# Optimization experiments

Hardware: AMD Instinct MI355X
Metric: run time of the kernel (lower is better)

The kernel has to match this reference:

```python
import jax, jax.numpy as jnp
import numpy as np

EPS_DIST = 1e-10
BN_EPS = 1e-5
K = 3  # nsample / three_nn


def setup_inputs() -> dict:
    key = jax.random.key(0)
    ks = jax.random.split(key, 8)
    B, N, S, D1, D2 = 4, 8192, 2048, 128, 256
    C_in = D1 + D2  # 384
    H = 256
    inp = {
        "pos1": jax.random.normal(ks[0], (B, 3, N), dtype=jnp.float32),
        "pos2": jax.random.normal(ks[1], (B, 3, S), dtype=jnp.float32),
        "feature1": jax.random.normal(ks[2], (B, D1, N), dtype=jnp.float32),
        "feature2": jax.random.normal(ks[3], (B, D2, S), dtype=jnp.float32),
        # MLP layer 1: Conv1d(384->256, k=1) + BN
        "W1": jax.random.normal(ks[4], (H, C_in), dtype=jnp.float32) * (1.0 / np.sqrt(C_in)),
        "b1": jnp.zeros((H,), dtype=jnp.float32),
        "g1": jnp.ones((H,), dtype=jnp.float32),
        "be1": jnp.zeros((H,), dtype=jnp.float32),
        # MLP layer 2: Conv1d(256->256, k=1) + BN
        "W2": jax.random.normal(ks[5], (H, H), dtype=jnp.float32) * (1.0 / np.sqrt(H)),
        "b2": jnp.zeros((H,), dtype=jnp.float32),
        "g2": jnp.ones((H,), dtype=jnp.float32),
        "be2": jnp.zeros((H,), dtype=jnp.float32),
    }
    return inp


def _conv_bn_relu(x, W, b, gamma, beta):
    # x: [B, Cin, N]; 1x1 Conv1d == channel GEMM
    y = jnp.einsum("oc,bcn->bon", W, x) + b[None, :, None]
    # BatchNorm1d in training mode: batch statistics over (B, N)
    mean = jnp.mean(y, axis=(0, 2), keepdims=True)
    var = jnp.mean(jnp.square(y - mean), axis=(0, 2), keepdims=True)
    y = (y - mean) * jax.lax.rsqrt(var + BN_EPS)
    y = y * gamma[None, :, None] + beta[None, :, None]
    return jax.nn.relu(y)


def reference(pos1, pos2, feature1, feature2, W1, b1, g1, be1, W2, b2, g2, be2):
    # pos1: [B,3,N], pos2: [B,3,S], feature1: [B,D1,N], feature2: [B,D2,S]
    p1 = jnp.swapaxes(pos1, 1, 2)  # [B,N,3]
    p2 = jnp.swapaxes(pos2, 1, 2)  # [B,S,3]
    # three_nn: squared-distance 3-NN of each point in p1 among p2
    d2 = (jnp.sum(p1 * p1, -1)[:, :, None]
          + jnp.sum(p2 * p2, -1)[:, None, :]
          - 2.0 * jnp.einsum("bnc,bsc->bns", p1, p2))  # [B,N,S]
    neg_vals, idx = jax.lax.top_k(-d2, K)  # idx: [B,N,3]
    dists = jnp.maximum(-neg_vals, EPS_DIST)  # dists[dists<1e-10]=1e-10
    w = 1.0 / dists
    w = w / jnp.sum(w, -1, keepdims=True)  # [B,N,3]
    # grouping_operation: gather feature2 [B,D,S] by idx -> [B,D,N,3]
    grouped = jax.vmap(lambda f, i: f[:, i])(feature2, idx)
    interpolated = jnp.sum(grouped * w[:, None, :, :], axis=-1)  # [B,D2,N]
    feat = jnp.concatenate([interpolated, feature1], axis=1)  # [B,384,N]
    feat = _conv_bn_relu(feat, W1, b1, g1, be1)
    feat = _conv_bn_relu(feat, W2, b2, g2, be2)
    return feat  # [B,256,N]
```

## Files before the change

### kernel.cpp

```cpp
#include <hip/hip_runtime.h>
#include <hip/hip_bf16.h>
#include <cstdint>

typedef unsigned short u16;
typedef unsigned int u32;
typedef unsigned long long u64;
typedef __bf16 bf16x8 __attribute__((ext_vector_type(8)));
typedef float f32x4 __attribute__((ext_vector_type(4)));

__device__ __forceinline__ u16 f2b(float f) {
    unsigned int u = __float_as_uint(f);
    u += 0x7fffu + ((u >> 16) & 1u);
    return (u16)(u >> 16);
}
__device__ __forceinline__ float b2f(u16 h) {
    return __uint_as_float(((unsigned int)h) << 16);
}
__device__ __forceinline__ void async_cp16(void* lds, const void* g) {
    __builtin_amdgcn_global_load_lds((const __attribute__((address_space(1))) void*)g,
                                     (__attribute__((address_space(3))) void*)lds, 16, 0, 0);
}
__device__ __forceinline__ u32 fmono(float f) {
    u32 u = __float_as_uint(f);
    return u ^ (((u32)((int)u >> 31)) | 0x80000000u);
}
__device__ __forceinline__ u64 shfl_xor_u64(u64 v, int mask) {
    u32 lo = (u32)v, hi = (u32)(v >> 32);
    lo = (u32)__shfl_xor((int)lo, mask);
    hi = (u32)__shfl_xor((int)hi, mask);
    return ((u64)hi << 32) | lo;
}
__device__ __forceinline__ void ins3(u64 k, u64& k0, u64& k1, u64& k2) {
    bool c0 = k > k0, c1 = k > k1, c2 = k > k2;
    k2 = c1 ? k1 : (c2 ? k : k2);
    k1 = c0 ? k0 : (c1 ? k : k1);
    k0 = c0 ? k : k0;
}
__device__ __forceinline__ int pkix(int i) { return i + (i >> 7); }

#define NB_NN  1024
#define NB_CVT 160
#define NB_T2  512
#define NB_T1  1024

__global__ __launch_bounds__(256, 8) void prep_kernel(const float* __restrict__ w1,
                                                      const float* __restrict__ w2,
                                                      u16* __restrict__ wb,
                                                      const float* __restrict__ feature2,
                                                      u16* __restrict__ f2t,
                                                      const float* __restrict__ feature1,
                                                      u16* __restrict__ f1t,
                                                      const float* __restrict__ pos1,
                                                      const float* __restrict__ pos2,
                                                      int* __restrict__ idx_out,
                                                      float* __restrict__ w_out) {
    __shared__ __align__(16) char smem[19712];
    int bi = blockIdx.x;
    int tid = threadIdx.x;

    if (bi >= NB_NN) {
        int ci = bi - NB_NN;
        if (ci < NB_CVT) {
            int i = ci * 256 + tid;
            if (i < 40960) {
                const float* src = (i < 24576) ? w1 : w2;
                int k = (i < 24576) ? i : (i - 24576);
                float4 v = *(const float4*)&src[(size_t)k * 4];
                ushort4 o;
                o.x = f2b(v.x); o.y = f2b(v.y); o.z = f2b(v.z); o.w = f2b(v.w);
                *(ushort4*)&wb[(size_t)i * 4] = o;
            }
            return;
        }
        float (*t)[65] = (float (*)[65])smem;
        const float* in; u16* out; int C, S, s0, c0, b;
        if (ci < NB_CVT + NB_T2) {
            int lin = ci - NB_CVT;
            C = 256; S = 2048; in = feature2; out = f2t;
            s0 = (lin & 31) * 64; c0 = ((lin >> 5) & 3) * 64; b = lin >> 7;
        } else {
            int lin = ci - NB_CVT - NB_T2;
            C = 128; S = 8192; in = feature1; out = f1t;
            s0 = (lin & 127) * 64; c0 = ((lin >> 7) & 1) * 64; b = lin >> 8;
        }
        const float* ib = in + (size_t)b * C * S;
        u16* ob = out + (size_t)b * S * C;
        int col = tid & 63, r0 = tid >> 6;
#pragma unroll
        for (int p = 0; p < 16; ++p) {
            int c = p * 4 + r0;
            t[c][col] = ib[(size_t)(c0 + c) * S + s0 + col];
        }
        __syncthreads();
#pragma unroll
        for (int p = 0; p < 16; ++p) {
            int s = p * 4 + r0;
            ob[(size_t)(s0 + s) * C + c0 + col] = f2b(t[col][s]);
        }
        return;
    }

    float4* pk = (float4*)smem;
    u64* warr = (u64*)(smem + 16512);
    int j0 = bi * 32;
    int b = j0 >> 13;
    const float* p2 = pos2 + (size_t)b * 3 * 2048;
    int p = tid & 15, ck = tid >> 4;
    int wv = tid >> 6, lane = tid & 63;
    int na = (j0 & 8191) + p, nbq = na + 16;
    const float* p1 = pos1 + (size_t)b * 3 * 8192;
    float xa = p1[na], ya = p1[8192 + na], za = p1[16384 + na];
    float xb = p1[nbq], yb = p1[8192 + nbq], zb = p1[16384 + nbq];

    u64 a0k = 0, a1k = 0, a2k = 0, b0k = 0, b1k = 0, b2k = 0;

    for (int half = 0; half < 2; ++half) {
        int hbase = half * 1024;
        for (int i = tid; i < 1024; i += 256) {
            int s = hbase + i;
            float x = p2[s], y = p2[2048 + s], z = p2[4096 + s];
            pk[pkix(i)] = make_float4(x, y, z, -0.5f * (x * x + y * y + z * z));
        }
        __syncthreads();

        float ga0 = -3.4e38f, ga1 = -3.4e38f, ga2 = -3.4e38f;
        float gb0 = -3.4e38f, gb1 = -3.4e38f, gb2 = -3.4e38f;
        int ia0 = 0, ia1 = 0, ia2 = 0, ib0 = 0, ib1 = 0, ib2 = 0;
        int sb = ck * 64;
        const float4* pc = pk + pkix(sb);
#pragma unroll 4
        for (int it = 0; it < 64; ++it) {
            float4 cd = pc[it];
            int s = sb + it;
            float ta = fmaf(xa, cd.x, fmaf(ya, cd.y, fmaf(za, cd.z, cd.w)));
            float tb = fmaf(xb, cd.x, fmaf(yb, cd.y, fmaf(zb, cd.z, cd.w)));
            bool a0 = ta > ga0, a1 = ta > ga1, a2 = ta > ga2;
            ga2 = a1 ? ga1 : (a2 ? ta : ga2);
            ia2 = a1 ? ia1 : (a2 ? s : ia2);
            ga1 = a0 ? ga0 : (a1 ? ta : ga1);
            ia1 = a0 ? ia0 : (a1 ? s : ia1);
            ga0 = a0 ? ta : ga0;
            ia0 = a0 ? s : ia0;
            bool b0c = tb > gb0, b1c = tb > gb1, b2c = tb > gb2;
            gb2 = b1c ? gb1 : (b2c ? tb : gb2);
            ib2 = b1c ? ib1 : (b2c ? s : ib2);
            gb1 = b0c ? gb0 : (b1c ? tb : gb1);
            ib1 = b0c ? ib0 : (b1c ? s : ib1);
            gb0 = b0c ? tb : gb0;
            ib0 = b0c ? s : ib0;
        }
        __syncthreads();

        int gi0 = hbase + ia0, gi1 = hbase + ia1, gi2 = hbase + ia2;
        int gj0 = hbase + ib0, gj1 = hbase + ib1, gj2 = hbase + ib2;
        ins3(((u64)fmono(ga0) << 32) | (u64)(2047 - gi0), a0k, a1k, a2k);
        ins3(((u64)fmono(ga1) << 32) | (u64)(2047 - gi1), a0k, a1k, a2k);
        ins3(((u64)fmono(ga2) << 32) | (u64)(2047 - gi2), a0k, a1k, a2k);
        ins3(((u64)fmono(gb0) << 32) | (u64)(2047 - gj0), b0k, b1k, b2k);
        ins3(((u64)fmono(gb1) << 32) | (u64)(2047 - gj1), b0k, b1k, b2k);
        ins3(((u64)fmono(gb2) << 32) | (u64)(2047 - gj2), b0k, b1k, b2k);
    }

#pragma unroll
    for (int mask = 16; mask <= 32; mask <<= 1) {
        u64 pa0 = shfl_xor_u64(a0k, mask), pa1 = shfl_xor_u64(a1k, mask), pa2 = shfl_xor_u64(a2k, mask);
        u64 pb0 = shfl_xor_u64(b0k, mask), pb1 = shfl_xor_u64(b1k, mask), pb2 = shfl_xor_u64(b2k, mask);
        ins3(pa0, a0k, a1k, a2k); ins3(pa1, a0k, a1k, a2k); ins3(pa2, a0k, a1k, a2k);
        ins3(pb0, b0k, b1k, b2k); ins3(pb1, b0k, b1k, b2k); ins3(pb2, b0k, b1k, b2k);
    }
    if (lane < 16) {
        u64* wr = &warr[(wv * 16 + p) * 6];
        wr[0] = a0k; wr[1] = a1k; wr[2] = a2k;
        wr[3] = b0k; wr[4] = b1k; wr[5] = b2k;
    }
    __syncthreads();
    if (tid < 32) {
        int q = tid;
        int pp = q & 15, off = (q < 16) ? 0 : 3;
        const u64* w0 = &warr[pp * 6];
        u64 k0 = w0[off], k1 = w0[off + 1], k2 = w0[off + 2];
#pragma unroll
        for (int w = 1; w < 4; ++w) {
            const u64* wr = &warr[(w * 16 + pp) * 6];
            ins3(wr[off], k0, k1, k2);
            ins3(wr[off + 1], k0, k1, k2);
            ins3(wr[off + 2], k0, k1, k2);
        }
        int s0 = 2047 - (int)(k0 & 0xFFFFFFFFu);
        int s1 = 2047 - (int)(k1 & 0xFFFFFFFFu);
        int s2 = 2047 - (int)(k2 & 0xFFFFFFFFu);
        int j = j0 + q;
        int n = j & 8191;
        float x1 = p1[n], y1 = p1[8192 + n], z1 = p1[16384 + n];
        float n1 = x1 * x1 + y1 * y1 + z1 * z1;
        float X0 = p2[s0], Y0 = p2[2048 + s0], Z0 = p2[4096 + s0];
        float X1 = p2[s1], Y1v = p2[2048 + s1], Z1 = p2[4096 + s1];
        float X2 = p2[s2], Y2v = p2[2048 + s2], Z2 = p2[4096 + s2];
        float t0 = x1 * X0 + y1 * Y0 + z1 * Z0 - 0.5f * (X0 * X0 + Y0 * Y0 + Z0 * Z0);
        float t1 = x1 * X1 + y1 * Y1v + z1 * Z1 - 0.5f * (X1 * X1 + Y1v * Y1v + Z1 * Z1);
        float t2 = x1 * X2 + y1 * Y2v + z1 * Z2 - 0.5f * (X2 * X2 + Y2v * Y2v + Z2 * Z2);
        float d0 = fmaxf(fmaf(-2.f, t0, n1), 1e-10f);
        float d1 = fmaxf(fmaf(-2.f, t1, n1), 1e-10f);
        float d2 = fmaxf(fmaf(-2.f, t2, n1), 1e-10f);
        float w0v = 1.f / d0, w1v = 1.f / d1, w2v = 1.f / d2;
        float inv = 1.f / (w0v + w1v + w2v);
        idx_out[j * 3] = s0; idx_out[j * 3 + 1] = s1; idx_out[j * 3 + 2] = s2;
        w_out[j * 3] = w0v * inv; w_out[j * 3 + 1] = w1v * inv; w_out[j * 3 + 2] = w2v * inv;
    }
}

__global__ __launch_bounds__(256) void gather_kernel(const u16* __restrict__ f2t,
                                                     const int* __restrict__ idx,
                                                     const float* __restrict__ wgt,
                                                     u16* __restrict__ interp) {
    int wv = threadIdx.x >> 6, lane = threadIdx.x & 63;
    int j = blockIdx.x * 4 + wv;
    int b = j >> 13;
    int i0 = idx[j * 3], i1 = idx[j * 3 + 1], i2 = idx[j * 3 + 2];
    float w0 = wgt[j * 3], w1 = wgt[j * 3 + 1], w2 = wgt[j * 3 + 2];
    const u16* r0 = f2t + ((size_t)(b * 2048 + i0)) * 256;
    const u16* r1 = f2t + ((size_t)(b * 2048 + i1)) * 256;
    const u16* r2 = f2t + ((size_t)(b * 2048 + i2)) * 256;
    int c = lane * 4;
    ushort4 v0 = *(const ushort4*)(r0 + c);
    ushort4 v1 = *(const ushort4*)(r1 + c);
    ushort4 v2 = *(const ushort4*)(r2 + c);
    ushort4 o;
    o.x = f2b(w0 * b2f(v0.x) + w1 * b2f(v1.x) + w2 * b2f(v2.x));
    o.y = f2b(w0 * b2f(v0.y) + w1 * b2f(v1.y) + w2 * b2f(v2.y));
    o.z = f2b(w0 * b2f(v0.z) + w1 * b2f(v1.z) + w2 * b2f(v2.z));
    o.w = f2b(w0 * b2f(v0.w) + w1 * b2f(v1.w) + w2 * b2f(v2.w));
    *(ushort4*)(interp + (size_t)j * 256 + c) = o;
}

template <int KT, bool SPLIT>
__global__ __launch_bounds__(256, 2) void gemm_kernel(const u16* __restrict__ A1,
                                                      const u16* __restrict__ A2,
                                                      const u16* __restrict__ Bw,
                                                      const float* __restrict__ bias,
                                                      u16* __restrict__ Yb,
                                                      float* __restrict__ stats) {
    __shared__ u16 Al[128 * 64];
    __shared__ u16 Bl[128 * 64];
    int tid = threadIdx.x;
    int lane = tid & 63, wv = tid >> 6;
    int j0 = blockIdx.x * 128, m0 = blockIdx.y * 128;
    int l15 = lane & 15, q = lane >> 4;
    int wj = (wv >> 1) * 64, wm = (wv & 1) * 64;
    f32x4 acc[4][4];
#pragma unroll
    for (int i = 0; i < 4; ++i)
#pragma unroll
        for (int jj = 0; jj < 4; ++jj) acc[i][jj] = (f32x4){0.f, 0.f, 0.f, 0.f};

    int rbase = wv * 32;
    int lrow = lane >> 3, lchunk = lane & 7;
    const u16* Bg = Bw + (size_t)m0 * KT;

    for (int k0 = 0; k0 < KT; k0 += 64) {
        const u16* src; int stride;
        if (!SPLIT || k0 < 256) { src = A1 + (size_t)j0 * 256 + k0; stride = 256; }
        else                    { src = A2 + (size_t)j0 * 128 + (k0 - 256); stride = 128; }
#pragma unroll
        for (int qq = 0; qq < 4; ++qq) {
            int row = rbase + qq * 8;
            async_cp16(&Al[row * 64], src + (size_t)(row + lrow) * stride + lchunk * 8);
            async_cp16(&Bl[row * 64], Bg + (size_t)(row + lrow) * KT + k0 + lchunk * 8);
        }
        __syncthreads();
#pragma unroll
        for (int ks = 0; ks < 2; ++ks) {
            bf16x8 af[4], bfr[4];
#pragma unroll
            for (int i = 0; i < 4; ++i)
                af[i] = *(const bf16x8*)&Al[(wj + i * 16 + l15) * 64 + ks * 32 + q * 8];
#pragma unroll
            for (int i = 0; i < 4; ++i)
                bfr[i] = *(const bf16x8*)&Bl[(wm + i * 16 + l15) * 64 + ks * 32 + q * 8];
#pragma unroll
            for (int i = 0; i < 4; ++i)
#pragma unroll
                for (int jj = 0; jj < 4; ++jj)
                    acc[i][jj] = __builtin_amdgcn_mfma_f32_16x16x32_bf16(af[i], bfr[jj],
                                                                         acc[i][jj], 0, 0, 0);
        }
        __syncthreads();
    }
#pragma unroll
    for (int jj = 0; jj < 4; ++jj) {
        int m = m0 + wm + jj * 16 + l15;
        float bv = bias[m];
        float s = 0.f, s2 = 0.f;
#pragma unroll
        for (int i = 0; i < 4; ++i) {
            int jr = j0 + wj + i * 16 + q * 4;
#pragma unroll
            for (int r = 0; r < 4; ++r) {
                float v = acc[i][jj][r] + bv;
                s += v; s2 += v * v;
                Yb[(size_t)(jr + r) * 256 + m] = f2b(v);
            }
        }
        s += __shfl_xor(s, 16); s += __shfl_xor(s, 32);
        s2 += __shfl_xor(s2, 16); s2 += __shfl_xor(s2, 32);
        if (q == 0) {
            atomicAdd(&stats[m], s);
            atomicAdd(&stats[256 + m], s2);
        }
    }
}

__global__ __launch_bounds__(256) void apply1_kernel(const u16* __restrict__ Y1,
                                                     const float* __restrict__ stats,
                                                     const float* __restrict__ g,
                                                     const float* __restrict__ be,
                                                     u16* __restrict__ X2) {
    size_t i = ((size_t)blockIdx.x * 256 + threadIdx.x) * 4;
    int m = (int)(i & 255);
    float4 sm = *(const float4*)&stats[m];
    float4 sq = *(const float4*)&stats[256 + m];
    float4 gg = *(const float4*)&g[m];
    float4 bb = *(const float4*)&be[m];
    const float inv = 1.f / 32768.f;
    float mean, var, aa[4], ss[4];
    mean = sm.x * inv; var = sq.x * inv - mean * mean; aa[0] = gg.x * rsqrtf(var + 1e-5f); ss[0] = bb.x - mean * aa[0];
    mean = sm.y * inv; var = sq.y * inv - mean * mean; aa[1] = gg.y * rsqrtf(var + 1e-5f); ss[1] = bb.y - mean * aa[1];
    mean = sm.z * inv; var = sq.z * inv - mean * mean; aa[2] = gg.z * rsqrtf(var + 1e-5f); ss[2] = bb.z - mean * aa[2];
    mean = sm.w * inv; var = sq.w * inv - mean * mean; aa[3] = gg.w * rsqrtf(var + 1e-5f); ss[3] = bb.w - mean * aa[3];
    ushort4 v = *(const ushort4*)&Y1[i];
    ushort4 o;
    o.x = f2b(fmaxf(b2f(v.x) * aa[0] + ss[0], 0.f));
    o.y = f2b(fmaxf(b2f(v.y) * aa[1] + ss[1], 0.f));
    o.z = f2b(fmaxf(b2f(v.z) * aa[2] + ss[2], 0.f));
    o.w = f2b(fmaxf(b2f(v.w) * aa[3] + ss[3], 0.f));
    *(ushort4*)&X2[i] = o;
}

__global__ __launch_bounds__(256) void final_out_kernel(const u16* __restrict__ Y2,
                                                        const float* __restrict__ stats,
                                                        const float* __restrict__ g,
                                                        const float* __restrict__ be,
                                                        float* __restrict__ out) {
    __shared__ float t[64][65];
    int j0 = blockIdx.x * 64, o0 = blockIdx.y * 64;
    int tid = threadIdx.x;
    int c4 = (tid & 15) * 4, rw = tid >> 4;
#pragma unroll
    for (int p = 0; p < 4; ++p) {
        int jl = p * 16 + rw;
        ushort4 v = *(const ushort4*)&Y2[(size_t)(j0 + jl) * 256 + o0 + c4];
        t[jl][c4] = b2f(v.x); t[jl][c4 + 1] = b2f(v.y);
        t[jl][c4 + 2] = b2f(v.z); t[jl][c4 + 3] = b2f(v.w);
    }
    __syncthreads();
    int b = j0 >> 13, n0 = j0 & 8191;
    const float inv = 1.f / 32768.f;
#pragma unroll
    for (int p = 0; p < 4; ++p) {
        int ol = p * 16 + rw;
        int o = o0 + ol;
        float mean = stats[o] * inv;
        float var = stats[256 + o] * inv - mean * mean;
        float a = g[o] * rsqrtf(var + 1e-5f);
        float s = be[o] - mean * a;
        float4 v;
        v.x = fmaxf(t[c4][ol] * a + s, 0.f);
        v.y = fmaxf(t[c4 + 1][ol] * a + s, 0.f);
        v.z = fmaxf(t[c4 + 2][ol] * a + s, 0.f);
        v.w = fmaxf(t[c4 + 3][ol] * a + s, 0.f);
        *(float4*)&out[(size_t)b * 2097152 + (size_t)o * 8192 + n0 + c4] = v;
    }
}

extern "C" void kernel_launch(void* const* d_in, const int* in_sizes, int n_in,
                              void* d_out, int out_size, void* d_ws, size_t ws_size,
                              hipStream_t stream) {
    const float* pos1 = (const float*)d_in[0];
    const float* pos2 = (const float*)d_in[1];
    const float* feature1 = (const float*)d_in[2];
    const float* feature2 = (const float*)d_in[3];
    const float* W1 = (const float*)d_in[4];
    const float* b1 = (const float*)d_in[5];
    const float* g1 = (const float*)d_in[6];
    const float* be1 = (const float*)d_in[7];
    const float* W2 = (const float*)d_in[8];
    const float* b2 = (const float*)d_in[9];
    const float* g2 = (const float*)d_in[10];
    const float* be2 = (const float*)d_in[11];

    char* ws = (char*)d_ws;
    int*   IDX    = (int*)(ws + 0);
    float* WGT    = (float*)(ws + 393216);
    u16*   W1B    = (u16*)(ws + 786432);
    u16*   W2B    = (u16*)(ws + 983040);
    float* STATS  = (float*)(ws + 1114112);
    u16*   F2T    = (u16*)(ws + 1118208);
    u16*   F1T    = (u16*)(ws + 5312512);
    u16*   INTERP = (u16*)(ws + 13701120);
    u16*   Y1     = (u16*)(ws + 30478336);
    u16*   X2     = (u16*)(ws + 47255552);
    u16*   Y2     = (u16*)(ws + 64032768);
    float* OUT    = (float*)d_out;

    hipMemsetAsync(STATS, 0, 1024 * sizeof(float), stream);
    prep_kernel<<<NB_NN + NB_CVT + NB_T2 + NB_T1, 256, 0, stream>>>(
        W1, W2, W1B, feature2, F2T, feature1, F1T, pos1, pos2, IDX, WGT);
    gather_kernel<<<8192, 256, 0, stream>>>(F2T, IDX, WGT, INTERP);
    gemm_kernel<384, true><<<dim3(256, 2), 256, 0, stream>>>(INTERP, F1T, W1B, b1, Y1, STATS);
    apply1_kernel<<<8192, 256, 0, stream>>>(Y1, STATS, g1, be1, X2);
    gemm_kernel<256, false><<<dim3(256, 2), 256, 0, stream>>>(X2, nullptr, W2B, b2, Y2, STATS + 512);
    final_out_kernel<<<dim3(512, 4), 256, 0, stream>>>(Y2, STATS + 512, g2, be2, OUT);
}
```

Before: 209.0 us.

## Fuse BN1 apply and ReLU into second GEMM's A-tile load; repad NN LDS

Measured after the change: 204.6 us. -2.1%, faster.

```diff
diff --git a/kernel.cpp b/kernel.cpp
--- a/kernel.cpp
+++ b/kernel.cpp
@@ -7,6 +7,7 @@
 typedef unsigned long long u64;
 typedef __bf16 bf16x8 __attribute__((ext_vector_type(8)));
 typedef float f32x4 __attribute__((ext_vector_type(4)));
+typedef u16 u16x8 __attribute__((ext_vector_type(8)));
 
 __device__ __forceinline__ u16 f2b(float f) {
     unsigned int u = __float_as_uint(f);
@@ -36,7 +37,7 @@
     k1 = c0 ? k0 : (c1 ? k : k1);
     k0 = c0 ? k : k0;
 }
-__device__ __forceinline__ int pkix(int i) { return i + (i >> 7); }
+__device__ __forceinline__ int pkix(int i) { return i + (i >> 6); }
 
 #define NB_NN  1024
 #define NB_CVT 160
@@ -101,7 +102,7 @@
     }
 
     float4* pk = (float4*)smem;
-    u64* warr = (u64*)(smem + 16512);
+    u64* warr = (u64*)(smem + 16640);
     int j0 = bi * 32;
     int b = j0 >> 13;
     const float* p2 = pos2 + (size_t)b * 3 * 2048;
@@ -233,11 +234,14 @@
     *(ushort4*)(interp + (size_t)j * 256 + c) = o;
 }
 
-template <int KT, bool SPLIT>
+template <int KT, bool SPLIT, bool FUSE>
 __global__ __launch_bounds__(256, 2) void gemm_kernel(const u16* __restrict__ A1,
                                                       const u16* __restrict__ A2,
                                                       const u16* __restrict__ Bw,
                                                       const float* __restrict__ bias,
+                                                      const float* __restrict__ stats_in,
+                                                      const float* __restrict__ g_in,
+                                                      const float* __restrict__ be_in,
                                                       u16* __restrict__ Yb,
                                                       float* __restrict__ stats) {
     __shared__ u16 Al[128 * 64];
@@ -258,14 +262,43 @@
     const u16* Bg = Bw + (size_t)m0 * KT;
 
     for (int k0 = 0; k0 < KT; k0 += 64) {
-        const u16* src; int stride;
-        if (!SPLIT || k0 < 256) { src = A1 + (size_t)j0 * 256 + k0; stride = 256; }
-        else                    { src = A2 + (size_t)j0 * 128 + (k0 - 256); stride = 128; }
-#pragma unroll
-        for (int qq = 0; qq < 4; ++qq) {
-            int row = rbase + qq * 8;
-            async_cp16(&Al[row * 64], src + (size_t)(row + lrow) * stride + lchunk * 8);
-            async_cp16(&Bl[row * 64], Bg + (size_t)(row + lrow) * KT + k0 + lchunk * 8);
+        if (FUSE) {
+            int c = k0 + lchunk * 8;
+            const float inv = 1.f / 32768.f;
+            float aa[8], ssv[8];
+#pragma unroll
+            for (int e = 0; e < 8; e += 4) {
+                float4 sm = *(const float4*)&stats_in[c + e];
+                float4 sq = *(const float4*)&stats_in[256 + c + e];
+                float4 gg = *(const float4*)&g_in[c + e];
+                float4 bb = *(const float4*)&be_in[c + e];
+                float m, v;
+                m = sm.x * inv; v = sq.x * inv - m * m; aa[e + 0] = gg.x * rsqrtf(v + 1e-5f); ssv[e + 0] = bb.x - m * aa[e + 0];
+                m = sm.y * inv; v = sq.y * inv - m * m; aa[e + 1] = gg.y * rsqrtf(v + 1e-5f); ssv[e + 1] = bb.y - m * aa[e + 1];
+                m = sm.z * inv; v = sq.z * inv - m * m; aa[e + 2] = gg.z * rsqrtf(v + 1e-5f); ssv[e + 2] = bb.z - m * aa[e + 2];
+                m = sm.w * inv; v = sq.w * inv - m * m; aa[e + 3] = gg.w * rsqrtf(v + 1e-5f); ssv[e + 3] = bb.w - m * aa[e + 3];
+            }
+#pragma unroll
+            for (int qq = 0; qq < 4; ++qq) {
+                int row = rbase + qq * 8;
+                u16x8 y = *(const u16x8*)&A1[(size_t)(j0 + row + lrow) * 256 + c];
+                u16x8 o;
+#pragma unroll
+                for (int e = 0; e < 8; ++e)
+                    o[e] = f2b(fmaxf(b2f(y[e]) * aa[e] + ssv[e], 0.f));
+                *(u16x8*)&Al[(row + lrow) * 64 + lchunk * 8] = o;
+                async_cp16(&Bl[row * 64], Bg + (size_t)(row + lrow) * KT + k0 + lchunk * 8);
+            }
+        } else {
+            const u16* src; int stride;
+            if (!SPLIT || k0 < 256) { src = A1 + (size_t)j0 * 256 + k0; stride = 256; }
+            else                    { src = A2 + (size_t)j0 * 128 + (k0 - 256); stride = 128; }
+#pragma unroll
+            for (int qq = 0; qq < 4; ++qq) {
+                int row = rbase + qq * 8;
+                async_cp16(&Al[row * 64], src + (size_t)(row + lrow) * stride + lchunk * 8);
+                async_cp16(&Bl[row * 64], Bg + (size_t)(row + lrow) * KT + k0 + lchunk * 8);
+            }
         }
         __syncthreads();
 #pragma unroll
@@ -308,32 +341,6 @@
             atomicAdd(&stats[256 + m], s2);
         }
     }
-}
-
-__global__ __launch_bounds__(256) void apply1_kernel(const u16* __restrict__ Y1,
-                                                     const float* __restrict__ stats,
-                                                     const float* __restrict__ g,
-                                                     const float* __restrict__ be,
-                                                     u16* __restrict__ X2) {
-    size_t i = ((size_t)blockIdx.x * 256 + threadIdx.x) * 4;
-    int m = (int)(i & 255);
-    float4 sm = *(const float4*)&stats[m];
-    float4 sq = *(const float4*)&stats[256 + m];
-    float4 gg = *(const float4*)&g[m];
-    float4 bb = *(const float4*)&be[m];
-    const float inv = 1.f / 32768.f;
-    float mean, var, aa[4], ss[4];
-    mean = sm.x * inv; var = sq.x * inv - mean * mean; aa[0] = gg.x * rsqrtf(var + 1e-5f); ss[0] = bb.x - mean * aa[0];
-    mean = sm.y * inv; var = sq.y * inv - mean * mean; aa[1] = gg.y * rsqrtf(var + 1e-5f); ss[1] = bb.y - mean * aa[1];
-    mean = sm.z * inv; var = sq.z * inv - mean * mean; aa[2] = gg.z * rsqrtf(var + 1e-5f); ss[2] = bb.z - mean * aa[2];
-    mean = sm.w * inv; var = sq.w * inv - mean * mean; aa[3] = gg.w * rsqrtf(var + 1e-5f); ss[3] = bb.w - mean * aa[3];
-    ushort4 v = *(const ushort4*)&Y1[i];
-    ushort4 o;
-    o.x = f2b(fmaxf(b2f(v.x) * aa[0] + ss[0], 0.f));
-    o.y = f2b(fmaxf(b2f(v.y) * aa[1] + ss[1], 0.f));
-    o.z = f2b(fmaxf(b2f(v.z) * aa[2] + ss[2], 0.f));
-    o.w = f2b(fmaxf(b2f(v.w) * aa[3] + ss[3], 0.f));
-    *(ushort4*)&X2[i] = o;
 }
 
 __global__ __launch_bounds__(256) void final_out_kernel(const u16* __restrict__ Y2,
@@ -398,16 +405,16 @@
     u16*   F1T    = (u16*)(ws + 5312512);
     u16*   INTERP = (u16*)(ws + 13701120);
     u16*   Y1     = (u16*)(ws + 30478336);
-    u16*   X2     = (u16*)(ws + 47255552);
-    u16*   Y2     = (u16*)(ws + 64032768);
+    u16*   Y2     = (u16*)(ws + 47255552);
     float* OUT    = (float*)d_out;
 
     hipMemsetAsync(STATS, 0, 1024 * sizeof(float), stream);
     prep_kernel<<<NB_NN + NB_CVT + NB_T2 + NB_T1, 256, 0, stream>>>(
         W1, W2, W1B, feature2, F2T, feature1, F1T, pos1, pos2, IDX, WGT);
     gather_kernel<<<8192, 256, 0, stream>>>(F2T, IDX, WGT, INTERP);
-    gemm_kernel<384, true><<<dim3(256, 2), 256, 0, stream>>>(INTERP, F1T, W1B, b1, Y1, STATS);
-    apply1_kernel<<<8192, 256, 0, stream>>>(Y1, STATS, g1, be1, X2);
-    gemm_kernel<256, false><<<dim3(256, 2), 256, 0, stream>>>(X2, nullptr, W2B, b2, Y2, STATS + 512);
+    gemm_kernel<384, true, false><<<dim3(256, 2), 256, 0, stream>>>(
+        INTERP, F1T, W1B, b1, nullptr, nullptr, nullptr, Y1, STATS);
+    gemm_kernel<256, false, true><<<dim3(256, 2), 256, 0, stream>>>(
+        Y1, nullptr, W2B, b2, STATS, g1, be1, Y2, STATS + 512);
     final_out_kernel<<<dim3(512, 4), 256, 0, stream>>>(Y2, STATS + 512, g2, be2, OUT);
 }
```
